# Optimization experiments

Measured on AMD Instinct MI355X. Metric: run time of the kernel, lower is better.

Reference implementation:

```python
import jax, jax.numpy as jnp
import numpy as np


def setup_inputs() -> dict:
    key = jax.random.key(0)
    ks = jax.random.split(key, 13)
    B, W, C = 16, 2048, 512
    inp = {
        "X_sfr": jax.random.normal(ks[0], (B, W, C), dtype=jnp.float32),
        "adj_matrix": jax.random.normal(ks[1], (B, C, C), dtype=jnp.float32),
        "log_temp": jnp.zeros((1,), dtype=jnp.float32),
        "wq": jax.random.normal(ks[2], (1,), dtype=jnp.float32),
        "bq": jax.random.normal(ks[3], (1,), dtype=jnp.float32),
        "wk": jax.random.normal(ks[4], (1,), dtype=jnp.float32),
        "bk": jax.random.normal(ks[5], (1,), dtype=jnp.float32),
        "wv": jax.random.normal(ks[6], (1,), dtype=jnp.float32),
        "bv": jax.random.normal(ks[7], (1,), dtype=jnp.float32),
        "wmu": jax.random.normal(ks[8], (1,), dtype=jnp.float32),
        "bmu": jax.random.normal(ks[9], (1,), dtype=jnp.float32),
        "wsig": jax.random.normal(ks[10], (1,), dtype=jnp.float32),
        "bsig": jax.random.normal(ks[11], (1,), dtype=jnp.float32),
        "k1": 20,
        "k2": 30,
    }
    return inp


def reference(X_sfr, adj_matrix, log_temp, wq, bq, wk, bk, wv, bv, wmu, bmu, wsig, bsig, k1, k2):
    B, W, C = X_sfr.shape
    # spatial propagation: relu + in-degree normalize adjacency
    adj_nonneg = jnp.maximum(adj_matrix, 0.0)
    in_deg = jnp.clip(adj_nonneg.sum(axis=1, keepdims=True), 1e-4)  # [B,1,C]
    adj_norm = adj_nonneg / in_deg
    X_spatial = jnp.einsum('bwi,bij->bwj', X_sfr, adj_norm)  # [B,W,C]

    # static band mask over time: k1 <= |dt| <= k2, fallback to identity rows
    t = jnp.arange(W)
    delta = jnp.abs(t[None, :] - t[:, None])
    band = (delta >= k1) & (delta <= k2)  # [W,W]
    has_valid = band.any(axis=1)
    band = jnp.where(has_valid[:, None], band, jnp.eye(W, dtype=bool))

    # scalar (1->1) q/k/v projections on the temporal token
    temporal_token = X_spatial.mean(axis=2, keepdims=True)  # [B,W,1]
    q = wq * temporal_token + bq                            # [B,W,1]
    k = wk * temporal_token + bk                            # [B,W,1]
    v = wv * X_spatial + bv                                 # [B,W,C]

    temp = jax.nn.softplus(log_temp)[0] + 1e-4
    logits = jnp.matmul(q, jnp.swapaxes(k, 1, 2)) / temp    # [B,W,W] rank-1
    logits = jnp.where(band[None, :, :], logits, -1e9)
    attn = jax.nn.softmax(logits, axis=-1)
    attn = attn * band[None, :, :].astype(attn.dtype)
    attn = attn / (attn.sum(axis=-1, keepdims=True) + 1e-6)

    sacon_scalar = attn.sum(axis=-1, keepdims=True)         # [B,W,1]
    sacon = jnp.broadcast_to(sacon_scalar, (B, W, C))

    X_temporal = jnp.matmul(attn, v)                        # [B,W,C]
    X_fused = X_temporal + X_spatial

    mu = jnp.clip(wmu * X_fused + bmu, -20.0, 20.0)
    sigma_sq = jax.nn.softplus(wsig * X_fused + bsig) + 0.1
    return mu, sigma_sq, sacon
```

## Files before the change

### kernel.cpp

```cpp
#include <hip/hip_runtime.h>
#include <math.h>

#define B_ 16
#define W_ 2048
#define C_ 512

#define OFF_XB    0
#define OFF_BT    33554432
#define OFF_XSP   41943040
#define OFF_TT    75497472

typedef short v8s __attribute__((ext_vector_type(8)));
typedef float v4f __attribute__((ext_vector_type(4)));
typedef unsigned int u32;

__device__ __forceinline__ float softplusf(float x) {
    return fmaxf(x, 0.f) + log1pf(expf(-fabsf(x)));
}
__device__ __forceinline__ unsigned short f2bf(float x) {
    unsigned int u = __float_as_uint(x);
    unsigned int r = (u + 0x7FFFu + ((u >> 16) & 1u)) >> 16;
    return (unsigned short)r;
}
__device__ __forceinline__ float bf2f(unsigned int h) {
    return __uint_as_float(h << 16);
}
__device__ __forceinline__ void gload16(const ushort* g, ushort* l) {
    __builtin_amdgcn_global_load_lds(
        (const __attribute__((address_space(1))) u32*)(g),
        (__attribute__((address_space(3))) u32*)(l), 16, 0, 0);
}

__global__ __launch_bounds__(256) void prep_adj(const float* __restrict__ adj,
                                                ushort* __restrict__ Bt) {
    __shared__ float cs[8][32];
    __shared__ float inv[32];
    __shared__ float t[32][33];
    const int b = blockIdx.y, j0 = blockIdx.x * 32;
    const int tx = threadIdx.x & 31, ty = threadIdx.x >> 5;
    const float* src = adj + (size_t)b * C_ * C_;

    float s = 0.f;
#pragma unroll 4
    for (int it = 0; it < C_ / 8; it++)
        s += fmaxf(src[(size_t)(it * 8 + ty) * C_ + j0 + tx], 0.f);
    cs[ty][tx] = s;
    __syncthreads();
    if (ty == 0) {
        float tot = cs[0][tx] + cs[1][tx] + cs[2][tx] + cs[3][tx]
                  + cs[4][tx] + cs[5][tx] + cs[6][tx] + cs[7][tx];
        inv[tx] = 1.f / fmaxf(tot, 1e-4f);
    }

    const int jr = threadIdx.x >> 4;
    const int ic = (threadIdx.x & 15) * 2;
    for (int i0t = 0; i0t < C_; i0t += 32) {
        __syncthreads();
#pragma unroll
        for (int rr = 0; rr < 4; rr++) {
            int ii = ty + rr * 8;
            t[ii][tx] = fmaxf(src[(size_t)(i0t + ii) * C_ + j0 + tx], 0.f);
        }
        __syncthreads();
#pragma unroll
        for (int pp = 0; pp < 2; pp++) {
            int j = jr + pp * 16;
            float iv = inv[j];
            ushort2 o;
            o.x = f2bf(t[ic][j] * iv);
            o.y = f2bf(t[ic + 1][j] * iv);
            *(ushort2*)&Bt[(size_t)b * C_ * C_ + (size_t)(j0 + j) * C_ + i0t + ic] = o;
        }
    }
}

__global__ void convertA(const float* __restrict__ X, ushort* __restrict__ Xb) {
    int idx = blockIdx.x * 256 + threadIdx.x;
    float4 v = ((const float4*)X)[idx];
    ushort4 o;
    o.x = f2bf(v.x); o.y = f2bf(v.y); o.z = f2bf(v.z); o.w = f2bf(v.w);
    ((ushort4*)Xb)[idx] = o;
}

__global__ __launch_bounds__(256) void gemm_mfma(const ushort* __restrict__ Xb,
                                                 const ushort* __restrict__ Bt,
                                                 ushort* __restrict__ Xsp,
                                                 float* __restrict__ tt) {
    __shared__ ushort As[128 * 32];
    __shared__ ushort Bs[128 * 32];
    const int b  = blockIdx.z;
    const int m0 = blockIdx.y * 128;
    const int n0 = blockIdx.x * 128;
    const int tid  = threadIdx.x;
    const int wave = tid >> 6, lane = tid & 63;
    const int quad = lane >> 4, l16 = lane & 15;
    const int mw = (wave & 1) * 64, nw = (wave >> 1) * 64;

    const ushort* Ag = Xb + (size_t)b * W_ * C_ + (size_t)m0 * C_;
    const ushort* Bg = Bt + (size_t)b * C_ * C_ + (size_t)n0 * C_;

    const int sm = tid >> 2;
    const int sk = (tid & 3) * 8;

    v4f acc[4][4];
#pragma unroll
    for (int mt = 0; mt < 4; mt++)
#pragma unroll
        for (int nt = 0; nt < 4; nt++)
            acc[mt][nt] = (v4f){0.f, 0.f, 0.f, 0.f};

    for (int k0 = 0; k0 < C_; k0 += 32) {
        __syncthreads();
        gload16(Ag + (size_t)sm * C_ + k0 + sk,        As + tid * 8);
        gload16(Ag + (size_t)(sm + 64) * C_ + k0 + sk, As + 2048 + tid * 8);
        gload16(Bg + (size_t)sm * C_ + k0 + sk,        Bs + tid * 8);
        gload16(Bg + (size_t)(sm + 64) * C_ + k0 + sk, Bs + 2048 + tid * 8);
        __syncthreads();

        v8s af[4], bf[4];
#pragma unroll
        for (int mt = 0; mt < 4; mt++)
            af[mt] = *(const v8s*)&As[(mw + mt * 16 + l16) * 32 + quad * 8];
#pragma unroll
        for (int nt = 0; nt < 4; nt++)
            bf[nt] = *(const v8s*)&Bs[(nw + nt * 16 + l16) * 32 + quad * 8];
#pragma unroll
        for (int mt = 0; mt < 4; mt++)
#pragma unroll
            for (int nt = 0; nt < 4; nt++)
                acc[mt][nt] = __builtin_amdgcn_mfma_f32_16x16x32_bf16(af[mt], bf[nt], acc[mt][nt], 0, 0, 0);
    }

#pragma unroll
    for (int mt = 0; mt < 4; mt++) {
#pragma unroll
        for (int nt = 0; nt < 4; nt++) {
            int col = n0 + nw + nt * 16 + l16;
#pragma unroll
            for (int r = 0; r < 4; r++) {
                int row = m0 + mw + mt * 16 + quad * 4 + r;
                Xsp[((size_t)b * W_ + row) * C_ + col] = f2bf(acc[mt][nt][r]);
            }
        }
    }

#pragma unroll
    for (int mt = 0; mt < 4; mt++) {
#pragma unroll
        for (int r = 0; r < 4; r++) {
            float s = acc[mt][0][r] + acc[mt][1][r] + acc[mt][2][r] + acc[mt][3][r];
            s += __shfl_xor(s, 1);
            s += __shfl_xor(s, 2);
            s += __shfl_xor(s, 4);
            s += __shfl_xor(s, 8);
            if (l16 == 0) {
                int row = m0 + mw + mt * 16 + quad * 4 + r;
                atomicAdd(&tt[b * W_ + row], s);
            }
        }
    }
}

__global__ __launch_bounds__(256) void final_kernel(const ushort* __restrict__ Xsp,
                                                    const float* __restrict__ tt,
                                                    const float* __restrict__ ltp,
                                                    const float* __restrict__ wqp, const float* __restrict__ bqp,
                                                    const float* __restrict__ wkp, const float* __restrict__ bkp,
                                                    const float* __restrict__ wvp, const float* __restrict__ bvp,
                                                    const float* __restrict__ wmup, const float* __restrict__ bmup,
                                                    const float* __restrict__ wsigp, const float* __restrict__ bsigp,
                                                    const int* __restrict__ k1p, const int* __restrict__ k2p,
                                                    float* __restrict__ out) {
    __shared__ float wlds[4][4][40];
    __shared__ float Ssh[4][4];
    const int wid = threadIdx.x >> 6, lane = threadIdx.x & 63;
    const int i0w = blockIdx.x * 16 + wid * 4;
    const int b = i0w >> 11, ib = i0w & (W_ - 1);
    const int K1 = k1p[0], K2 = k2p[0];
    int ns = K2 - K1 + 1;
    if (ns > 16) ns = 16;
    const int n2 = 2 * ns;
    const int nsL = ns + 3;
    const int nu = 2 * nsL;

    for (int k = threadIdx.x; k < 4 * 4 * 40; k += 256) ((float*)wlds)[k] = 0.f;
    __syncthreads();

    if (lane < 32) {
        const float cinv = 1.f / C_;
        const float temp = softplusf(ltp[0]) + 1e-4f;
        const float invt = 1.f / temp;
        const float wkc = wkp[0] * cinv, bk = bkp[0];
        const float wqc = wqp[0] * cinv, bq = bqp[0];
        const float* ttb = tt + b * W_;
        for (int r = 0; r < 4; r++) {
            const int i = ib + r;
            const float q = wqc * ttb[i] + bq;
            int s = lane;
            int j = (s < ns) ? (i - K2 + s) : (i + K1 + (s - ns));
            bool valid = (s < n2) && (j >= 0) && (j < W_);
            float l = valid ? (q * (wkc * ttb[j] + bk) * invt) : -INFINITY;
            float mx = l;
#pragma unroll
            for (int off = 16; off > 0; off >>= 1) mx = fmaxf(mx, __shfl_xor(mx, off, 32));
            float e = valid ? expf(l - mx) : 0.f;
            float T = e;
#pragma unroll
            for (int off = 16; off > 0; off >>= 1) T += __shfl_xor(T, off, 32);
            float p = e / T;
            float S = p;
#pragma unroll
            for (int off = 16; off > 0; off >>= 1) S += __shfl_xor(S, off, 32);
            float rn = 1.f / (S + 1e-6f);
            if (s < n2) {
                int u = (s < ns) ? (r + s) : (nsL + r + (s - ns));
                wlds[wid][r][u] = p * rn;
            }
            if (lane == 0) Ssh[wid][r] = S * rn;
        }
    }
    __syncthreads();

    const ushort* Xbp = Xsp + (size_t)b * W_ * C_;
    const int c8 = lane * 8;
    float acc[4][8];
#pragma unroll
    for (int r = 0; r < 4; r++)
#pragma unroll
        for (int k = 0; k < 8; k++) acc[r][k] = 0.f;

    for (int u = 0; u < nu; u++) {
        int j = (u < nsL) ? (ib - K2 + u) : (ib + K1 + (u - nsL));
        j = min(max(j, 0), W_ - 1);
        uint4 v = *(const uint4*)(Xbp + (size_t)j * C_ + c8);
        float x[8];
        x[0] = bf2f(v.x & 0xffff); x[1] = bf2f(v.x >> 16);
        x[2] = bf2f(v.y & 0xffff); x[3] = bf2f(v.y >> 16);
        x[4] = bf2f(v.z & 0xffff); x[5] = bf2f(v.z >> 16);
        x[6] = bf2f(v.w & 0xffff); x[7] = bf2f(v.w >> 16);
#pragma unroll
        for (int r = 0; r < 4; r++) {
            float w = wlds[wid][r][u];
#pragma unroll
            for (int k = 0; k < 8; k++) acc[r][k] = fmaf(w, x[k], acc[r][k]);
        }
    }

    const float wv = wvp[0], bv = bvp[0];
    const float wmu = wmup[0], bmu = bmup[0];
    const float wsig = wsigp[0], bsig = bsigp[0];
    const size_t N = (size_t)B_ * W_ * C_;

#pragma unroll
    for (int r = 0; r < 4; r++) {
        const float S = Ssh[wid][r];
        uint4 xv = *(const uint4*)(Xbp + (size_t)(ib + r) * C_ + c8);
        float xs[8];
        xs[0] = bf2f(xv.x & 0xffff); xs[1] = bf2f(xv.x >> 16);
        xs[2] = bf2f(xv.y & 0xffff); xs[3] = bf2f(xv.y >> 16);
        xs[4] = bf2f(xv.z & 0xffff); xs[5] = bf2f(xv.z >> 16);
        xs[6] = bf2f(xv.w & 0xffff); xs[7] = bf2f(xv.w >> 16);

        float mu[8], sg[8];
#pragma unroll
        for (int k = 0; k < 8; k++) {
            float xf = fmaf(wv, acc[r][k], bv * S) + xs[k];
            mu[k] = fminf(fmaxf(fmaf(wmu, xf, bmu), -20.f), 20.f);
            sg[k] = softplusf(fmaf(wsig, xf, bsig)) + 0.1f;
        }

        const size_t base = (size_t)(i0w + r) * C_ + c8;
        *(float4*)&out[base]     = (float4){mu[0], mu[1], mu[2], mu[3]};
        *(float4*)&out[base + 4] = (float4){mu[4], mu[5], mu[6], mu[7]};
        *(float4*)&out[N + base]     = (float4){sg[0], sg[1], sg[2], sg[3]};
        *(float4*)&out[N + base + 4] = (float4){sg[4], sg[5], sg[6], sg[7]};
        *(float4*)&out[2 * N + base]     = (float4){S, S, S, S};
        *(float4*)&out[2 * N + base + 4] = (float4){S, S, S, S};
    }
}

extern "C" void kernel_launch(void* const* d_in, const int* in_sizes, int n_in,
                              void* d_out, int out_size, void* d_ws, size_t ws_size,
                              hipStream_t stream) {
    const float* X_sfr = (const float*)d_in[0];
    const float* adj   = (const float*)d_in[1];
    const float* ltp   = (const float*)d_in[2];
    const float* wq    = (const float*)d_in[3];
    const float* bq    = (const float*)d_in[4];
    const float* wk    = (const float*)d_in[5];
    const float* bk    = (const float*)d_in[6];
    const float* wv    = (const float*)d_in[7];
    const float* bv    = (const float*)d_in[8];
    const float* wmu   = (const float*)d_in[9];
    const float* bmu   = (const float*)d_in[10];
    const float* wsig  = (const float*)d_in[11];
    const float* bsig  = (const float*)d_in[12];
    const int*   k1p   = (const int*)d_in[13];
    const int*   k2p   = (const int*)d_in[14];

    char* ws = (char*)d_ws;
    ushort* Xb  = (ushort*)(ws + OFF_XB);
    ushort* Bt  = (ushort*)(ws + OFF_BT);
    ushort* Xsp = (ushort*)(ws + OFF_XSP);
    float*  tt  = (float*)(ws + OFF_TT);
    float*  out = (float*)d_out;

    hipMemsetAsync(tt, 0, B_ * W_ * sizeof(float), stream);

    prep_adj<<<dim3(C_ / 32, B_), 256, 0, stream>>>(adj, Bt);

    convertA<<<(B_ * W_ * C_ / 4) / 256, 256, 0, stream>>>(X_sfr, Xb);

    gemm_mfma<<<dim3(C_ / 128, W_ / 128, B_), 256, 0, stream>>>(Xb, Bt, Xsp, tt);

    final_kernel<<<(B_ * W_) / 16, 256, 0, stream>>>(Xsp, tt, ltp, wq, bq, wk, bk,
                                                     wv, bv, wmu, bmu, wsig, bsig,
                                                     k1p, k2p, out);
}
```

Measured before the change: 383.8 us.

## Single-pass adjacency prep, fold tt memset, skip zero weights, nontemporal output stores

prep_adj now reads each adjacency column stripe once into shared memory, using 512 threads, and computes both the column sums and the transposed bf16 output from that copy, instead of reading the adjacency twice. The separate memset of the temporal-token accumulator is moved into prep_adj, which removes one launch. In the final kernel, band weights that fall outside the valid range are written to LDS only when valid, and zero weights skip their FMAs. The three large outputs are written with nontemporal stores to reduce cache pollution. The 512x33 float stripe uses about 66 KB of LDS per block, which limits occupancy. The zero-weight branch adds divergence, and if the LDS weights are not cleared elsewhere, invalid slots may now hold stale values.

```diff
diff --git a/kernel.cpp b/kernel.cpp
--- a/kernel.cpp
+++ b/kernel.cpp
@@ -30,47 +30,52 @@
         (const __attribute__((address_space(1))) u32*)(g),
         (__attribute__((address_space(3))) u32*)(l), 16, 0, 0);
 }
-
-__global__ __launch_bounds__(256) void prep_adj(const float* __restrict__ adj,
-                                                ushort* __restrict__ Bt) {
-    __shared__ float cs[8][32];
+__device__ __forceinline__ void st_nt4(float* p, float a, float b, float c, float d) {
+    v4f v = {a, b, c, d};
+    __builtin_nontemporal_store(v, (v4f*)p);
+}
+
+__global__ __launch_bounds__(512) void prep_adj(const float* __restrict__ adj,
+                                                ushort* __restrict__ Bt,
+                                                float* __restrict__ tt) {
+    __shared__ float stripe[C_][33];
+    __shared__ float cs[16][32];
     __shared__ float inv[32];
-    __shared__ float t[32][33];
     const int b = blockIdx.y, j0 = blockIdx.x * 32;
-    const int tx = threadIdx.x & 31, ty = threadIdx.x >> 5;
-    const float* src = adj + (size_t)b * C_ * C_;
+    const int tid = threadIdx.x;
+    const int tx = tid & 31, ty = tid >> 5;
+    const float* src = adj + (size_t)b * C_ * C_ + j0;
+
+    if (tid < 128) tt[(blockIdx.y * 16 + blockIdx.x) * 128 + tid] = 0.f;
 
     float s = 0.f;
-#pragma unroll 4
-    for (int it = 0; it < C_ / 8; it++)
-        s += fmaxf(src[(size_t)(it * 8 + ty) * C_ + j0 + tx], 0.f);
+#pragma unroll 8
+    for (int it = 0; it < 32; it++) {
+        int row = it * 16 + ty;
+        float v = fmaxf(src[(size_t)row * C_ + tx], 0.f);
+        stripe[row][tx] = v;
+        s += v;
+    }
     cs[ty][tx] = s;
     __syncthreads();
     if (ty == 0) {
-        float tot = cs[0][tx] + cs[1][tx] + cs[2][tx] + cs[3][tx]
-                  + cs[4][tx] + cs[5][tx] + cs[6][tx] + cs[7][tx];
+        float tot = 0.f;
+#pragma unroll
+        for (int r = 0; r < 16; r++) tot += cs[r][tx];
         inv[tx] = 1.f / fmaxf(tot, 1e-4f);
     }
-
-    const int jr = threadIdx.x >> 4;
-    const int ic = (threadIdx.x & 15) * 2;
+    __syncthreads();
+
+    const int jr = tid >> 4;
+    const int ic = (tid & 15) * 2;
+    const float iv = inv[jr];
+    ushort* dst = Bt + (size_t)b * C_ * C_ + (size_t)(j0 + jr) * C_;
+#pragma unroll
     for (int i0t = 0; i0t < C_; i0t += 32) {
-        __syncthreads();
-#pragma unroll
-        for (int rr = 0; rr < 4; rr++) {
-            int ii = ty + rr * 8;
-            t[ii][tx] = fmaxf(src[(size_t)(i0t + ii) * C_ + j0 + tx], 0.f);
-        }
-        __syncthreads();
-#pragma unroll
-        for (int pp = 0; pp < 2; pp++) {
-            int j = jr + pp * 16;
-            float iv = inv[j];
-            ushort2 o;
-            o.x = f2bf(t[ic][j] * iv);
-            o.y = f2bf(t[ic + 1][j] * iv);
-            *(ushort2*)&Bt[(size_t)b * C_ * C_ + (size_t)(j0 + j) * C_ + i0t + ic] = o;
-        }
+        ushort2 o;
+        o.x = f2bf(stripe[i0t + ic][jr] * iv);
+        o.y = f2bf(stripe[i0t + ic + 1][jr] * iv);
+        *(ushort2*)&dst[i0t + ic] = o;
     }
 }
 
@@ -212,7 +217,7 @@
 #pragma unroll
             for (int off = 16; off > 0; off >>= 1) S += __shfl_xor(S, off, 32);
             float rn = 1.f / (S + 1e-6f);
-            if (s < n2) {
+            if (valid) {
                 int u = (s < ns) ? (r + s) : (nsL + r + (s - ns));
                 wlds[wid][r][u] = p * rn;
             }
@@ -241,8 +246,10 @@
 #pragma unroll
         for (int r = 0; r < 4; r++) {
             float w = wlds[wid][r][u];
-#pragma unroll
-            for (int k = 0; k < 8; k++) acc[r][k] = fmaf(w, x[k], acc[r][k]);
+            if (w != 0.f) {
+#pragma unroll
+                for (int k = 0; k < 8; k++) acc[r][k] = fmaf(w, x[k], acc[r][k]);
+            }
         }
     }
 
@@ -270,12 +277,12 @@
         }
 
         const size_t base = (size_t)(i0w + r) * C_ + c8;
-        *(float4*)&out[base]     = (float4){mu[0], mu[1], mu[2], mu[3]};
-        *(float4*)&out[base + 4] = (float4){mu[4], mu[5], mu[6], mu[7]};
-        *(float4*)&out[N + base]     = (float4){sg[0], sg[1], sg[2], sg[3]};
-        *(float4*)&out[N + base + 4] = (float4){sg[4], sg[5], sg[6], sg[7]};
-        *(float4*)&out[2 * N + base]     = (float4){S, S, S, S};
-        *(float4*)&out[2 * N + base + 4] = (float4){S, S, S, S};
+        st_nt4(&out[base],     mu[0], mu[1], mu[2], mu[3]);
+        st_nt4(&out[base + 4], mu[4], mu[5], mu[6], mu[7]);
+        st_nt4(&out[N + base],     sg[0], sg[1], sg[2], sg[3]);
+        st_nt4(&out[N + base + 4], sg[4], sg[5], sg[6], sg[7]);
+        st_nt4(&out[2 * N + base],     S, S, S, S);
+        st_nt4(&out[2 * N + base + 4], S, S, S, S);
     }
 }
 
@@ -305,9 +312,7 @@
     float*  tt  = (float*)(ws + OFF_TT);
     float*  out = (float*)d_out;
 
-    hipMemsetAsync(tt, 0, B_ * W_ * sizeof(float), stream);
-
-    prep_adj<<<dim3(C_ / 32, B_), 256, 0, stream>>>(adj, Bt);
+    prep_adj<<<dim3(C_ / 32, B_), 512, 0, stream>>>(adj, Bt, tt);
 
     convertA<<<(B_ * W_ * C_ / 4) / 256, 256, 0, stream>>>(X_sfr, Xb);
 
```

Result: slower. 396.9 us (+3.4%).
